# Kernel optimization log

Hardware: AMD Instinct MI355X
Metric: run time of the kernel (lower is better)

## Reference

```python
import jax, jax.numpy as jnp
import numpy as np

B, N, D = 8, 8192, 512
H, WIDTH = 8, 2048
DH = D // H
EPS = 1e-5


def _ln(x, g, b):
    m = jnp.mean(x, axis=-1, keepdims=True)
    v = jnp.mean(jnp.square(x - m), axis=-1, keepdims=True)
    return (x - m) * jax.lax.rsqrt(v + EPS) * g + b


def setup_inputs() -> dict:
    key = jax.random.key(0)
    ks = jax.random.split(key, 16)
    s = 0.02
    return {
        "x": jax.random.normal(ks[0], (B, N, D), dtype=jnp.float32),
        "mask": jnp.ones((B, N), dtype=jnp.float32),
        "Wq": jax.random.normal(ks[1], (D, D), dtype=jnp.float32) * s,
        "bq": jnp.zeros((D,), dtype=jnp.float32),
        "Wk": jax.random.normal(ks[2], (D, D), dtype=jnp.float32) * s,
        "bk": jnp.zeros((D,), dtype=jnp.float32),
        "Wv": jax.random.normal(ks[3], (D, D), dtype=jnp.float32) * s,
        "bv": jnp.zeros((D,), dtype=jnp.float32),
        "q_alpha": jax.random.normal(ks[4], (H, DH), dtype=jnp.float32),
        "k_beta": jax.random.normal(ks[5], (H, DH), dtype=jnp.float32),
        "Wo": jax.random.normal(ks[6], (D, D), dtype=jnp.float32) * s,
        "bo": jnp.zeros((D,), dtype=jnp.float32),
        "ln0_g": jnp.ones((D,), dtype=jnp.float32),
        "ln0_b": jnp.zeros((D,), dtype=jnp.float32),
        "ln1_g": jnp.ones((D,), dtype=jnp.float32),
        "ln1_b": jnp.zeros((D,), dtype=jnp.float32),
        "W1": jax.random.normal(ks[7], (WIDTH, D), dtype=jnp.float32) * s,
        "b1": jnp.zeros((WIDTH,), dtype=jnp.float32),
        "W2": jax.random.normal(ks[8], (D, WIDTH), dtype=jnp.float32) * s,
        "b2": jnp.zeros((D,), dtype=jnp.float32),
    }


def reference(x, mask, Wq, bq, Wk, bk, Wv, bv, q_alpha, k_beta, Wo, bo,
              ln0_g, ln0_b, ln1_g, ln1_b, W1, b1, W2, b2):
    scale = DH ** -0.5
    mask_ = mask[..., None]                       # [B,N,1]
    valid = (mask != 0)[..., None]                # [B,N,1] bool, broadcast over H

    residual = x
    xn = _ln(x, ln0_g, ln0_b) * mask_

    Q = (xn @ Wq.T + bq).reshape(B, N, H, DH)
    K = (xn @ Wk.T + bk).reshape(B, N, H, DH)
    V = (xn @ Wv.T + bv).reshape(B, N, H, DH)

    # stage 1: global query pooling
    alpha = jnp.einsum('bnhd,hd->bnh', Q, q_alpha) * scale
    alpha = jnp.where(valid, alpha, -jnp.inf)
    alpha = jax.nn.softmax(alpha, axis=1)         # softmax over N
    global_q = jnp.einsum('bnhd,bnh->bhd', Q, alpha)

    # stage 2: global value pooling
    P = K * global_q[:, None]                     # [B,N,H,DH]
    beta = jnp.einsum('bnhd,hd->bnh', P, k_beta) * scale
    beta = jnp.where(valid, beta, -jnp.inf)
    beta = jax.nn.softmax(beta, axis=1)
    global_v = jnp.einsum('bnhd,bnh->bhd', V, beta)

    out = (Q + global_v[:, None]).reshape(B, N, D)
    out = out @ Wo.T + bo
    x = residual + out

    residual = x
    xn = _ln(x, ln1_g, ln1_b)
    h = jax.nn.gelu(xn @ W1.T + b1, approximate=False)
    h = jax.nn.gelu(h @ W2.T + b2, approximate=False)
    x = residual + h
    x = x * mask_
    return x
```

## Files before the change

kernel.cpp:

```cpp
#include <hip/hip_runtime.h>
#include <hip/hip_bf16.h>
#include <math.h>

typedef short s8v __attribute__((ext_vector_type(8)));
typedef short s4v __attribute__((ext_vector_type(4)));
typedef __bf16 bf8v __attribute__((ext_vector_type(8)));
typedef float f4v __attribute__((ext_vector_type(4)));

#define GLOBAL_AS __attribute__((address_space(1)))
#define LDS_AS __attribute__((address_space(3)))

static __device__ __forceinline__ float bf2f(ushort u) {
  return __builtin_bit_cast(float, (unsigned int)u << 16);
}
static __device__ __forceinline__ ushort f2bf(float f) {
  unsigned int u = __builtin_bit_cast(unsigned int, f);
  u += 0x7FFFu + ((u >> 16) & 1u);
  return (ushort)(u >> 16);
}
static __device__ __forceinline__ float gelu_f(float v) {
  float t = v * v;
  float u = v * (0.0356774081f * t + 0.7978845608f);
  float e = __expf(-2.0f * u);
  return v * __builtin_amdgcn_rcpf(1.0f + e);
}
static __device__ __forceinline__ float wave_max_f(float v) {
  #pragma unroll
  for (int o = 32; o >= 1; o >>= 1) v = fmaxf(v, __shfl_xor(v, o));
  return v;
}
static __device__ __forceinline__ float wave_sum_f(float v) {
  #pragma unroll
  for (int o = 32; o >= 1; o >>= 1) v += __shfl_xor(v, o);
  return v;
}
static __device__ __forceinline__ void gload16(const ushort* g, const ushort* l) {
  __builtin_amdgcn_global_load_lds(
      (const GLOBAL_AS unsigned int*)g,
      (LDS_AS unsigned int*)l, 16, 0, 0);
}

__global__ void cvt_f32_bf16(const float* __restrict__ in, ushort* __restrict__ out, int n) {
  int i = (blockIdx.x * 256 + threadIdx.x) * 4;
  if (i >= n) return;
  float4 v = *(const float4*)(in + i);
  s4v o;
  o[0] = (short)f2bf(v.x); o[1] = (short)f2bf(v.y);
  o[2] = (short)f2bf(v.z); o[3] = (short)f2bf(v.w);
  *(s4v*)(out + i) = o;
}

__global__ __launch_bounds__(256) void transpose512(
    const float* __restrict__ in, float* __restrict__ out) {
  __shared__ float t[32][33];
  const int bx = blockIdx.x & 15, by = blockIdx.x >> 4;
  const int tx = threadIdx.x & 31, ty = threadIdx.x >> 5;
  #pragma unroll
  for (int i = 0; i < 4; ++i)
    t[ty + i * 8][tx] = in[(long)(by * 32 + ty + i * 8) * 512 + bx * 32 + tx];
  __syncthreads();
  #pragma unroll
  for (int i = 0; i < 4; ++i)
    out[(long)(bx * 32 + ty + i * 8) * 512 + by * 32 + tx] = t[tx][ty + i * 8];
}

__global__ __launch_bounds__(256) void wqo_kernel(
    const float* __restrict__ Wo, const float* __restrict__ Wq,
    ushort* __restrict__ WqoB)
{
  __shared__ float lO[64][33];
  __shared__ float lQ[32][65];
  const int t = threadIdx.x;
  const int bi = (blockIdx.x & 7) * 64, bj = (blockIdx.x >> 3) * 64;
  float acc[16] = {};
  for (int k0 = 0; k0 < 512; k0 += 32) {
    __syncthreads();
    {
      const int r = t >> 2, c = (t & 3) * 8;
      #pragma unroll
      for (int j = 0; j < 8; ++j) lO[r][c + j] = Wo[(long)(bi + r) * 512 + k0 + c + j];
      const int r2 = t >> 3, c2 = (t & 7) * 8;
      #pragma unroll
      for (int j = 0; j < 8; ++j) lQ[r2][c2 + j] = Wq[(long)(k0 + r2) * 512 + bj + c2 + j];
    }
    __syncthreads();
    const int j = t & 63, ig = t >> 6;
    for (int kk = 0; kk < 32; ++kk) {
      float q = lQ[kk][j];
      #pragma unroll
      for (int ii = 0; ii < 16; ++ii) acc[ii] += lO[ig * 16 + ii][kk] * q;
    }
  }
  const int j = t & 63, ig = t >> 6;
  #pragma unroll
  for (int ii = 0; ii < 16; ++ii)
    WqoB[(long)(bi + ig * 16 + ii) * 512 + bj + j] = f2bf(acc[ii]);
}

__global__ __launch_bounds__(256) void wa_kernel(
    const float* __restrict__ qa, const float* __restrict__ Wq,
    const float* __restrict__ bqv, ushort* __restrict__ waB, float* __restrict__ ca)
{
  __shared__ float ql[64];
  const int h = blockIdx.x;
  const int t = threadIdx.x;
  if (h >= 8) {
    waB[h * 512 + t] = 0; waB[h * 512 + 256 + t] = 0;
    if (t == 0) ca[h] = 0.f;
    return;
  }
  if (t < 64) ql[t] = qa[h * 64 + t];
  __syncthreads();
  #pragma unroll
  for (int half = 0; half < 2; ++half) {
    const int k = half * 256 + t;
    float s = 0;
    for (int dd = 0; dd < 64; ++dd) s += ql[dd] * Wq[(long)(h * 64 + dd) * 512 + k];
    waB[h * 512 + k] = f2bf(s);
  }
  if (t == 0) {
    float s = 0;
    for (int dd = 0; dd < 64; ++dd) s += ql[dd] * bqv[h * 64 + dd];
    ca[h] = s;
  }
}

__global__ __launch_bounds__(256) void ln_rows(
    const float* __restrict__ x, const float* __restrict__ gam,
    const float* __restrict__ bet, const float* __restrict__ mask,
    ushort* __restrict__ out)
{
  const int tid = threadIdx.x, lane = tid & 63, wv = tid >> 6;
  const long row = (long)blockIdx.x * 4 + wv;
  const float* xp = x + row * 512 + lane * 8;
  float4 a = *(const float4*)xp;
  float4 b = *(const float4*)(xp + 4);
  float s = a.x + a.y + a.z + a.w + b.x + b.y + b.z + b.w;
  float q = a.x*a.x + a.y*a.y + a.z*a.z + a.w*a.w
          + b.x*b.x + b.y*b.y + b.z*b.z + b.w*b.w;
  s = wave_sum_f(s); q = wave_sum_f(q);
  float m = s * (1.f / 512.f);
  float var = q * (1.f / 512.f) - m * m;
  float r = rsqrtf(var + 1e-5f);
  float mk = mask ? mask[row] : 1.f;
  const float* gp = gam + lane * 8;
  const float* bp = bet + lane * 8;
  float4 g0 = *(const float4*)gp, g1 = *(const float4*)(gp + 4);
  float4 c0 = *(const float4*)bp, c1 = *(const float4*)(bp + 4);
  s8v o;
  o[0] = (short)f2bf(((a.x - m) * r * g0.x + c0.x) * mk);
  o[1] = (short)f2bf(((a.y - m) * r * g0.y + c0.y) * mk);
  o[2] = (short)f2bf(((a.z - m) * r * g0.z + c0.z) * mk);
  o[3] = (short)f2bf(((a.w - m) * r * g0.w + c0.w) * mk);
  o[4] = (short)f2bf(((b.x - m) * r * g1.x + c1.x) * mk);
  o[5] = (short)f2bf(((b.y - m) * r * g1.y + c1.y) * mk);
  o[6] = (short)f2bf(((b.z - m) * r * g1.z + c1.z) * mk);
  o[7] = (short)f2bf(((b.w - m) * r * g1.w + c1.w) * mk);
  *(s8v*)(out + row * 512 + lane * 8) = o;
}

template<int BS, int CS>
__global__ __launch_bounds__(256) void logits_k(
    const ushort* __restrict__ XN, const ushort* __restrict__ Wl,
    const float* __restrict__ cvec, const float* __restrict__ mask,
    float* __restrict__ outL)
{
  __shared__ ushort lw[16 * 512];
  const int tid = threadIdx.x, lane = tid & 63, wv = tid >> 6;
  const long r0 = (long)blockIdx.x * 64;
  const int b = (int)(r0 >> 13);
  #pragma unroll
  for (int i = 0; i < 4; ++i) {
    const int u = tid + i * 256;
    const int h2 = u >> 6, uu = u & 63;
    s8v v = *(const s8v*)(Wl + (long)b * BS + h2 * 512 + uu * 8);
    *(s8v*)(lw + h2 * 512 + (uu ^ (h2 & 7)) * 8) = v;
  }
  __syncthreads();
  const int h = lane & 15, q = lane >> 4;
  const long rw = r0 + wv * 16;
  const ushort* ap = XN + (rw + (lane & 15)) * 512 + q * 8;
  f4v acc = {};
  #pragma unroll
  for (int t = 0; t < 16; ++t) {
    bf8v a = *(const bf8v*)(ap + t * 32);
    bf8v bb = *(const bf8v*)(lw + h * 512 + (((t * 4 + q) ^ (h & 7))) * 8);
    acc = __builtin_amdgcn_mfma_f32_16x16x32_bf16(a, bb, acc, 0, 0, 0);
  }
  const float cv = cvec[b * CS + h];
  #pragma unroll
  for (int j = 0; j < 4; ++j) {
    const long n = rw + q * 4 + j;
    float v = (acc[j] + cv) * 0.125f;
    if (mask[n] == 0.f) v = -1e30f;
    if (h < 8) outL[((long)((b << 3) + h) << 13) + (n & 8191)] = v;
  }
}

__global__ __launch_bounds__(1024) void softmax_rows(float* __restrict__ L)
{
  __shared__ float red[16];
  __shared__ float bc;
  const int tid = threadIdx.x, lane = tid & 63, wv = tid >> 6;
  float* p = L + ((long)blockIdx.x << 13) + tid * 8;
  float4 v0 = *(float4*)p;
  float4 v1 = *(float4*)(p + 4);
  float m = fmaxf(fmaxf(fmaxf(v0.x, v0.y), fmaxf(v0.z, v0.w)),
                  fmaxf(fmaxf(v1.x, v1.y), fmaxf(v1.z, v1.w)));
  m = wave_max_f(m);
  if (lane == 0) red[wv] = m;
  __syncthreads();
  if (tid < 64) {
    float t = (lane < 16) ? red[lane] : -INFINITY;
    t = wave_max_f(t);
    if (lane == 0) bc = t;
  }
  __syncthreads();
  const float gm = bc;
  v0.x = __expf(v0.x - gm); v0.y = __expf(v0.y - gm);
  v0.z = __expf(v0.z - gm); v0.w = __expf(v0.w - gm);
  v1.x = __expf(v1.x - gm); v1.y = __expf(v1.y - gm);
  v1.z = __expf(v1.z - gm); v1.w = __expf(v1.w - gm);
  float s = v0.x + v0.y + v0.z + v0.w + v1.x + v1.y + v1.z + v1.w;
  s = wave_sum_f(s);
  __syncthreads();
  if (lane == 0) red[wv] = s;
  __syncthreads();
  if (tid < 64) {
    float t = (lane < 16) ? red[lane] : 0.f;
    t = wave_sum_f(t);
    if (lane == 0) bc = t;
  }
  __syncthreads();
  const float inv = 1.0f / bc;
  v0.x *= inv; v0.y *= inv; v0.z *= inv; v0.w *= inv;
  v1.x *= inv; v1.y *= inv; v1.z *= inv; v1.w *= inv;
  *(float4*)p = v0;
  *(float4*)(p + 4) = v1;
}

__global__ __launch_bounds__(256) void pool_w(
    const ushort* __restrict__ XN, const float* __restrict__ wbuf,
    float* __restrict__ part)
{
  __shared__ float wlds[128][8];
  __shared__ float cmb[4][512];
  const int tid = threadIdx.x;
  const int b = blockIdx.x >> 6, ch = blockIdx.x & 63;
  const long g0 = ((long)b << 13) + ch * 128;
  if (tid < 128) {
    #pragma unroll
    for (int h = 0; h < 8; ++h)
      wlds[tid][h] = wbuf[(((long)(b * 8 + h)) << 13) + ch * 128 + tid];
  }
  __syncthreads();
  const int rg = tid >> 6, c8 = (tid & 63) * 8;
  f4v acc[8][2] = {};
  for (int it = 0; it < 32; ++it) {
    const int r = it * 4 + rg;
    s8v xv = *(const s8v*)(XN + (g0 + r) * 512 + c8);
    float xf[8];
    #pragma unroll
    for (int j = 0; j < 8; ++j) xf[j] = bf2f((ushort)xv[j]);
    #pragma unroll
    for (int h = 0; h < 8; ++h) {
      const float w = wlds[r][h];
      #pragma unroll
      for (int j = 0; j < 8; ++j) acc[h][j >> 2][j & 3] += w * xf[j];
    }
  }
  #pragma unroll
  for (int h = 0; h < 8; ++h) {
    __syncthreads();
    #pragma unroll
    for (int j = 0; j < 8; ++j) cmb[rg][c8 + j] = acc[h][j >> 2][j & 3];
    __syncthreads();
    const int col = tid * 2;
    float s0 = cmb[0][col] + cmb[1][col] + cmb[2][col] + cmb[3][col];
    float s1 = cmb[0][col + 1] + cmb[1][col + 1] + cmb[2][col + 1] + cmb[3][col + 1];
    *(float2*)(part + (((long)blockIdx.x * 8 + h) << 9) + col) = make_float2(s0, s1);
  }
}

__global__ __launch_bounds__(256) void combine_px(
    const float* __restrict__ part, float* __restrict__ px)
{
  const int bh = blockIdx.x;
  const int b = bh >> 3, h = bh & 7;
  const int col = threadIdx.x * 2;
  float s0 = 0.f, s1 = 0.f;
  for (int ch = 0; ch < 64; ++ch) {
    const float* p = part + (((long)((b * 64 + ch) * 8 + h)) << 9) + col;
    s0 += p[0]; s1 += p[1];
  }
  px[(bh << 9) + col] = s0;
  px[(bh << 9) + col + 1] = s1;
}

__global__ __launch_bounds__(64) void prep_gq_wb(
    const float* __restrict__ px, const float* __restrict__ WqT,
    const float* __restrict__ bqv, const float* __restrict__ kbv,
    const float* __restrict__ Wk, const float* __restrict__ bkv,
    ushort* __restrict__ wbB, float* __restrict__ cbs)
{
  __shared__ float pxl[512];
  __shared__ float gkb[64];
  const int bh = blockIdx.x, b = bh >> 3, h = bh & 7, d = threadIdx.x;
  #pragma unroll
  for (int i = 0; i < 8; ++i) pxl[d + i * 64] = px[(bh << 9) + d + i * 64];
  __syncthreads();
  float acc = bqv[h * 64 + d];
  for (int c = 0; c < 512; ++c) acc += pxl[c] * WqT[(long)c * 512 + h * 64 + d];
  gkb[d] = acc * kbv[h * 64 + d];
  __syncthreads();
  float s[8] = {};
  for (int dd = 0; dd < 64; ++dd) {
    const float g = gkb[dd];
    const float* wr = Wk + (long)(h * 64 + dd) * 512 + d;
    #pragma unroll
    for (int ki = 0; ki < 8; ++ki) s[ki] += g * wr[ki * 64];
  }
  #pragma unroll
  for (int ki = 0; ki < 8; ++ki)
    wbB[(long)(b * 16 + h) * 512 + d + ki * 64] = f2bf(s[ki]);
  if (d == 0) {
    float t = 0.f;
    for (int dd = 0; dd < 64; ++dd) t += gkb[dd] * bkv[h * 64 + dd];
    cbs[b * 16 + h] = t;
  }
  if (h == 0) {
    #pragma unroll
    for (int hp = 8; hp < 16; ++hp)
      for (int k = d; k < 512; k += 64) wbB[(long)(b * 16 + hp) * 512 + k] = 0;
    if (d < 8) cbs[b * 16 + 8 + d] = 0.f;
  }
}

__global__ __launch_bounds__(64) void prep_gv(
    const float* __restrict__ pv, const float* __restrict__ WvT,
    const float* __restrict__ bvv, const float* __restrict__ bqv,
    float* __restrict__ gvb)
{
  __shared__ float pxl[512];
  const int bh = blockIdx.x, b = bh >> 3, h = bh & 7, d = threadIdx.x;
  #pragma unroll
  for (int i = 0; i < 8; ++i) pxl[d + i * 64] = pv[(bh << 9) + d + i * 64];
  __syncthreads();
  float acc = bvv[h * 64 + d] + bqv[h * 64 + d];
  for (int c = 0; c < 512; ++c) acc += pxl[c] * WvT[(long)c * 512 + h * 64 + d];
  gvb[b * 512 + h * 64 + d] = acc;
}

__global__ __launch_bounds__(256) void bias_gv(
    const float* __restrict__ gv, const float* __restrict__ Wo,
    const float* __restrict__ bo, float* __restrict__ bo2) {
  const int b = blockIdx.x;
  const int n = blockIdx.y * 256 + threadIdx.x;
  const float* g = gv + b * 512;
  const float* w = Wo + (long)n * 512;
  float acc = 0.f;
  for (int d = 0; d < 512; d += 4) {
    float4 wv4 = *(const float4*)(w + d);
    acc += g[d] * wv4.x + g[d + 1] * wv4.y + g[d + 2] * wv4.z + g[d + 3] * wv4.w;
  }
  bo2[b * 512 + n] = bo[n] + acc;
}

#define MFMA_(d,a,b) d = __builtin_amdgcn_mfma_f32_16x16x32_bf16(a, b, d, 0, 0, 0)

template<int EPI, int LDA, int NN, int KK>
__global__ __launch_bounds__(512, 2) void gemm256(
    const ushort* __restrict__ A, const ushort* __restrict__ W,
    const float* __restrict__ bias, const float* __restrict__ resid,
    const float* __restrict__ mask, void* __restrict__ Out)
{
  constexpr int NBX = NN / 256;
  constexpr int NT = KK / 64;
  __shared__ __align__(16) ushort lds[2][2][16384];
  const int tid = threadIdx.x;
  const int lane = tid & 63;
  const int w = tid >> 6;
  const int wm = w >> 2, wn = w & 3;

  const int nwg = gridDim.x;
  const int cpx = nwg >> 3;
  const int wg = (blockIdx.x & 7) * cpx + (blockIdx.x >> 3);
  const int bx = wg % NBX, by = wg / NBX;
  const long bm = (long)by * 256;
  const int bn = bx * 256;

  const int srow = tid >> 3;
  const int sku = (tid & 7) ^ (srow & 7);
  const ushort* aln[4];
  const ushort* bln[4];
  #pragma unroll
  for (int l = 0; l < 4; ++l) {
    aln[l] = A + (bm + l * 64 + srow) * (long)LDA + sku * 8;
    bln[l] = W + (long)(bn + l * 64 + srow) * KK + sku * 8;
  }

#define STG_A(bf_, l_, Tt) gload16(aln[l_] + (Tt) * 64, &lds[bf_][0][(l_) * 4096 + w * 512])
#define STG_B(bf_, l_, Tt) gload16(bln[l_] + (Tt) * 64, &lds[bf_][1][(l_) * 4096 + w * 512])

  STG_B(0, 0, 0); STG_B(0, 1, 0);
  STG_B(0, 2, 0); STG_B(0, 3, 0);
  STG_A(0, 0, 0); STG_A(0, 2, 0);
  STG_A(0, 1, 0); STG_A(0, 3, 0);

  f4v acc[8][4] = {};

  const int s0 = ((lane >> 4) ^ (lane & 7)) * 8;
  const int s1 = ((4 + (lane >> 4)) ^ (lane & 7)) * 8;
  const int ar = (wm * 128 + (lane & 15)) * 64;
  const int br = (wn * 64 + (lane & 15)) * 64;

  asm volatile("s_waitcnt vmcnt(2)" ::: "memory");
  asm volatile("s_barrier" ::: "memory");

  for (int T = 0; T < NT; ++T) {
    const int buf = T & 1, nb = buf ^ 1;
    const ushort* LA = &lds[buf][0][0];
    const ushort* LB = &lds[buf][1][0];
    const bool st = (T + 1 < NT);
    bf8v aR[8], bR[8];
    #pragma unroll
    for (int m = 0; m < 4; ++m) {
      aR[2 * m]     = *(const bf8v*)(LA + ar + m * 1024 + s0);
      aR[2 * m + 1] = *(const bf8v*)(LA + ar + m * 1024 + s1);
    }
    #pragma unroll
    for (int n = 0; n < 2; ++n) {
      bR[2 * n]     = *(const bf8v*)(LB + br + n * 1024 + s0);
      bR[2 * n + 1] = *(const bf8v*)(LB + br + n * 1024 + s1);
    }
    if (st) { STG_B(nb, 0, T + 1); STG_B(nb, 1, T + 1); }
    asm volatile("s_barrier" ::: "memory");
    __builtin_amdgcn_s_setprio(1);
    #pragma unroll
    for (int m = 0; m < 4; ++m)
      #pragma unroll
      for (int n = 0; n < 2; ++n) {
        MFMA_(acc[m][n], aR[2 * m], bR[2 * n]);
        MFMA_(acc[m][n], aR[2 * m + 1], bR[2 * n + 1]);
      }
    __builtin_amdgcn_s_setprio(0);
    #pragma unroll
    for (int n = 2; n < 4; ++n) {
      bR[2 * n]     = *(const bf8v*)(LB + br + n * 1024 + s0);
      bR[2 * n + 1] = *(const bf8v*)(LB + br + n * 1024 + s1);
    }
    if (st) { STG_B(nb, 2, T + 1); STG_B(nb, 3, T + 1); }
    if (st) asm volatile("s_waitcnt vmcnt(4)" ::: "memory");
    else    asm volatile("s_waitcnt vmcnt(0)" ::: "memory");
    asm volatile("s_barrier" ::: "memory");
    __builtin_amdgcn_s_setprio(1);
    #pragma unroll
    for (int m = 0; m < 4; ++m)
      #pragma unroll
      for (int n = 2; n < 4; ++n) {
        MFMA_(acc[m][n], aR[2 * m], bR[2 * n]);
        MFMA_(acc[m][n], aR[2 * m + 1], bR[2 * n + 1]);
      }
    __builtin_amdgcn_s_setprio(0);
    #pragma unroll
    for (int m = 0; m < 4; ++m) {
      aR[2 * m]     = *(const bf8v*)(LA + ar + (m + 4) * 1024 + s0);
      aR[2 * m + 1] = *(const bf8v*)(LA + ar + (m + 4) * 1024 + s1);
    }
    if (st) { STG_A(nb, 0, T + 1); STG_A(nb, 2, T + 1); }
    asm volatile("s_barrier" ::: "memory");
    __builtin_amdgcn_s_setprio(1);
    #pragma unroll
    for (int m = 0; m < 4; ++m)
      #pragma unroll
      for (int n = 0; n < 2; ++n) {
        MFMA_(acc[m + 4][n], aR[2 * m], bR[2 * n]);
        MFMA_(acc[m + 4][n], aR[2 * m + 1], bR[2 * n + 1]);
      }
    __builtin_amdgcn_s_setprio(0);
    if (st) { STG_A(nb, 1, T + 1); STG_A(nb, 3, T + 1); }
    asm volatile("s_waitcnt vmcnt(2)" ::: "memory");
    asm volatile("s_barrier" ::: "memory");
    __builtin_amdgcn_s_setprio(1);
    #pragma unroll
    for (int m = 0; m < 4; ++m)
      #pragma unroll
      for (int n = 2; n < 4; ++n) {
        MFMA_(acc[m + 4][n], aR[2 * m], bR[2 * n]);
        MFMA_(acc[m + 4][n], aR[2 * m + 1], bR[2 * n + 1]);
      }
    __builtin_amdgcn_s_setprio(0);
  }
#undef STG_A
#undef STG_B

  const int colbase = bn + wn * 64 + (lane & 15);
  const long rowb0 = bm + wm * 128 + ((lane >> 4) * 4);
  const float* biasp = (EPI == 4) ? bias + ((bm >> 13) << 9) : bias;
  #pragma unroll
  for (int m = 0; m < 8; ++m) {
    #pragma unroll
    for (int j = 0; j < 4; ++j) {
      const long row = rowb0 + m * 16 + j;
      #pragma unroll
      for (int n = 0; n < 4; ++n) {
        const int col = colbase + n * 16;
        float v = acc[m][n][j] + biasp[col];
        const long idx = row * (long)NN + col;
        if constexpr (EPI == 0) {
          ((ushort*)Out)[idx] = f2bf(v);
        } else if constexpr (EPI == 2) {
          ((ushort*)Out)[idx] = f2bf(gelu_f(v));
        } else if constexpr (EPI == 3) {
          ((float*)Out)[idx] = (resid[idx] + gelu_f(v)) * mask[row];
        } else {
          ((float*)Out)[idx] = v + resid[idx];
        }
      }
    }
  }
}

extern "C" void kernel_launch(void* const* d_in, const int* in_sizes, int n_in,
                              void* d_out, int out_size, void* d_ws, size_t ws_size,
                              hipStream_t stream) {
  const float* x    = (const float*)d_in[0];
  const float* mask = (const float*)d_in[1];
  const float* Wq   = (const float*)d_in[2];
  const float* bq   = (const float*)d_in[3];
  const float* Wk   = (const float*)d_in[4];
  const float* bk   = (const float*)d_in[5];
  const float* Wv   = (const float*)d_in[6];
  const float* bv   = (const float*)d_in[7];
  const float* qa   = (const float*)d_in[8];
  const float* kb   = (const float*)d_in[9];
  const float* Wo   = (const float*)d_in[10];
  const float* bo   = (const float*)d_in[11];
  const float* g0   = (const float*)d_in[12];
  const float* be0  = (const float*)d_in[13];
  const float* g1   = (const float*)d_in[14];
  const float* be1  = (const float*)d_in[15];
  const float* W1   = (const float*)d_in[16];
  const float* b1   = (const float*)d_in[17];
  const float* W2   = (const float*)d_in[18];
  const float* b2   = (const float*)d_in[19];
  float* out = (float*)d_out;

  const int M = 65536;
  char* ws = (char*)d_ws;
  const size_t MB = 1024 * 1024;
  ushort* XN  = (ushort*)(ws);
  float*  X1  = (float*)(ws + 64 * MB);
  ushort* H1  = (ushort*)(ws + 192 * MB);
  float*  AL  = (float*)(ws + 192 * MB);
  float*  BL  = (float*)(ws + 194 * MB);
  float*  PART= (float*)(ws + 196 * MB);
  char* base = ws + 448 * MB;
  ushort* W1B  = (ushort*)(base);
  ushort* W2B  = (ushort*)(base + 2 * MB);
  ushort* WqoB = (ushort*)(base + 4 * MB);
  float*  WqT  = (float*)(base + 4 * MB + 512 * 1024);
  float*  WvT  = (float*)(base + 5 * MB + 512 * 1024);
  ushort* waB  = (ushort*)(base + 6 * MB + 512 * 1024);
  ushort* wbB  = (ushort*)(base + 6 * MB + 528 * 1024);
  float*  ca   = (float*)(base + 6 * MB + 656 * 1024);
  float*  cbs  = (float*)(base + 6 * MB + 660 * 1024);
  float*  PX   = (float*)(base + 6 * MB + 664 * 1024);
  float*  PV   = (float*)(base + 6 * MB + 792 * 1024);
  float*  GVB  = (float*)(base + 6 * MB + 920 * 1024);
  float*  BO2  = (float*)(base + 6 * MB + 936 * 1024);

  cvt_f32_bf16<<<1024, 256, 0, stream>>>(W1, W1B, 1048576);
  cvt_f32_bf16<<<1024, 256, 0, stream>>>(W2, W2B, 1048576);
  wqo_kernel<<<64, 256, 0, stream>>>(Wo, Wq, WqoB);
  wa_kernel<<<16, 256, 0, stream>>>(qa, Wq, bq, waB, ca);
  transpose512<<<256, 256, 0, stream>>>(Wq, WqT);
  transpose512<<<256, 256, 0, stream>>>(Wv, WvT);

  ln_rows<<<M / 4, 256, 0, stream>>>(x, g0, be0, mask, XN);

  logits_k<0, 0><<<1024, 256, 0, stream>>>(XN, waB, ca, mask, AL);
  softmax_rows<<<64, 1024, 0, stream>>>(AL);
  pool_w<<<512, 256, 0, stream>>>(XN, AL, PART);
  combine_px<<<64, 256, 0, stream>>>(PART, PX);
  prep_gq_wb<<<64, 64, 0, stream>>>(PX, WqT, bq, kb, Wk, bk, wbB, cbs);

  logits_k<8192, 16><<<1024, 256, 0, stream>>>(XN, wbB, cbs, mask, BL);
  softmax_rows<<<64, 1024, 0, stream>>>(BL);
  pool_w<<<512, 256, 0, stream>>>(XN, BL, PART);
  combine_px<<<64, 256, 0, stream>>>(PART, PV);
  prep_gv<<<64, 64, 0, stream>>>(PV, WvT, bv, bq, GVB);
  bias_gv<<<dim3(8, 2), 256, 0, stream>>>(GVB, Wo, bo, BO2);

  gemm256<4, 512, 512, 512><<<2 * (M / 256), 512, 0, stream>>>(
      XN, WqoB, BO2, x, nullptr, X1);

  ln_rows<<<M / 4, 256, 0, stream>>>(X1, g1, be1, nullptr, XN);

  gemm256<2, 512, 2048, 512><<<8 * (M / 256), 512, 0, stream>>>(
      XN, W1B, b1, nullptr, nullptr, H1);
  gemm256<3, 2048, 512, 2048><<<2 * (M / 256), 512, 0, stream>>>(
      H1, W2B, b2, X1, mask, out);
}
```

Baseline: 703.1 us.

## Shrink GEMM tiles to 128x256 with K=32 steps and store X1 as bf16

The three big GEMMs move from a 256x256 tile with K-step 64 and 64KB LDS to a 128x256 tile with K-step 32 and a single combined LDS buffer. Launch bounds now allow four workgroups per CU, aiming for higher occupancy and better latency hiding. The intermediate residual X1 is now stored as bf16 instead of fp32, with a new bf16 LayerNorm kernel, to cut memory traffic. In exchange, each loaded tile is reused less, there are more barriers per unit of work, and the residual path loses precision.

```diff
diff --git a/kernel.cpp b/kernel.cpp
--- a/kernel.cpp
+++ b/kernel.cpp
@@ -159,6 +159,35 @@
   *(s8v*)(out + row * 512 + lane * 8) = o;
 }
 
+__global__ __launch_bounds__(256) void ln_rows_bf16(
+    const ushort* __restrict__ x, const float* __restrict__ gam,
+    const float* __restrict__ bet, ushort* __restrict__ out)
+{
+  const int tid = threadIdx.x, lane = tid & 63, wv = tid >> 6;
+  const long row = (long)blockIdx.x * 4 + wv;
+  s8v v = *(const s8v*)(x + row * 512 + lane * 8);
+  float xv[8];
+  #pragma unroll
+  for (int j = 0; j < 8; ++j) xv[j] = bf2f((ushort)v[j]);
+  float s = 0.f, q = 0.f;
+  #pragma unroll
+  for (int j = 0; j < 8; ++j) { s += xv[j]; q += xv[j] * xv[j]; }
+  s = wave_sum_f(s); q = wave_sum_f(q);
+  float m = s * (1.f / 512.f);
+  float var = q * (1.f / 512.f) - m * m;
+  float r = rsqrtf(var + 1e-5f);
+  const float* gp = gam + lane * 8;
+  const float* bp = bet + lane * 8;
+  float4 g0 = *(const float4*)gp, g1 = *(const float4*)(gp + 4);
+  float4 c0 = *(const float4*)bp, c1 = *(const float4*)(bp + 4);
+  float gg[8] = {g0.x, g0.y, g0.z, g0.w, g1.x, g1.y, g1.z, g1.w};
+  float cc[8] = {c0.x, c0.y, c0.z, c0.w, c1.x, c1.y, c1.z, c1.w};
+  s8v o;
+  #pragma unroll
+  for (int j = 0; j < 8; ++j) o[j] = (short)f2bf((xv[j] - m) * r * gg[j] + cc[j]);
+  *(s8v*)(out + row * 512 + lane * 8) = o;
+}
+
 template<int BS, int CS>
 __global__ __launch_bounds__(256) void logits_k(
     const ushort* __restrict__ XN, const ushort* __restrict__ Wl,
@@ -369,14 +398,14 @@
 #define MFMA_(d,a,b) d = __builtin_amdgcn_mfma_f32_16x16x32_bf16(a, b, d, 0, 0, 0)
 
 template<int EPI, int LDA, int NN, int KK>
-__global__ __launch_bounds__(512, 2) void gemm256(
+__global__ __launch_bounds__(512, 4) void gemmP(
     const ushort* __restrict__ A, const ushort* __restrict__ W,
-    const float* __restrict__ bias, const float* __restrict__ resid,
+    const float* __restrict__ bias, const void* __restrict__ resid,
     const float* __restrict__ mask, void* __restrict__ Out)
 {
   constexpr int NBX = NN / 256;
-  constexpr int NT = KK / 64;
-  __shared__ __align__(16) ushort lds[2][2][16384];
+  constexpr int NT = KK / 32;
+  __shared__ __align__(16) ushort lds[2][12288];
   const int tid = threadIdx.x;
   const int lane = tid & 63;
   const int w = tid >> 6;
@@ -386,135 +415,93 @@
   const int cpx = nwg >> 3;
   const int wg = (blockIdx.x & 7) * cpx + (blockIdx.x >> 3);
   const int bx = wg % NBX, by = wg / NBX;
-  const long bm = (long)by * 256;
+  const long bm = (long)by * 128;
   const int bn = bx * 256;
 
-  const int srow = tid >> 3;
-  const int sku = (tid & 7) ^ (srow & 7);
-  const ushort* aln[4];
-  const ushort* bln[4];
-  #pragma unroll
-  for (int l = 0; l < 4; ++l) {
-    aln[l] = A + (bm + l * 64 + srow) * (long)LDA + sku * 8;
-    bln[l] = W + (long)(bn + l * 64 + srow) * KK + sku * 8;
-  }
-
-#define STG_A(bf_, l_, Tt) gload16(aln[l_] + (Tt) * 64, &lds[bf_][0][(l_) * 4096 + w * 512])
-#define STG_B(bf_, l_, Tt) gload16(bln[l_] + (Tt) * 64, &lds[bf_][1][(l_) * 4096 + w * 512])
-
-  STG_B(0, 0, 0); STG_B(0, 1, 0);
-  STG_B(0, 2, 0); STG_B(0, 3, 0);
-  STG_A(0, 0, 0); STG_A(0, 2, 0);
-  STG_A(0, 1, 0); STG_A(0, 3, 0);
-
-  f4v acc[8][4] = {};
-
-  const int s0 = ((lane >> 4) ^ (lane & 7)) * 8;
-  const int s1 = ((4 + (lane >> 4)) ^ (lane & 7)) * 8;
-  const int ar = (wm * 128 + (lane & 15)) * 64;
-  const int br = (wn * 64 + (lane & 15)) * 64;
-
-  asm volatile("s_waitcnt vmcnt(2)" ::: "memory");
+  const int scr = tid >> 2, sls = tid & 3;
+  const int akU = ((sls ^ (scr & 3) ^ ((scr >> 2) & 3))) * 8;
+  const ushort* asrc = A + (bm + scr) * (long)LDA + akU;
+  const int rbe = (scr & 31) + ((scr >> 5) << 6);
+  const ushort* besrc = W + (long)(bn + rbe) * KK + akU;
+  const ushort* bosrc = W + (long)(bn + rbe + 32) * KK + akU;
+
+#define STG_A(nb_, Tt)  gload16(asrc + (Tt) * 32, &lds[nb_][tid * 8])
+#define STG_BE(nb_, Tt) gload16(besrc + (Tt) * 32, &lds[nb_][4096 + tid * 8])
+#define STG_BO(nb_, Tt) gload16(bosrc + (Tt) * 32, &lds[nb_][8192 + tid * 8])
+
+  STG_A(0, 0); STG_BE(0, 0); STG_BO(0, 0);
+
+  f4v acc[4][4] = {};
+
+  const int L = lane & 15, q = lane >> 4;
+  const int soff = (q ^ (lane & 3) ^ ((lane >> 2) & 3)) * 8;
+  const int abase = (wm * 64 + L) * 32 + soff;
+  const int bbase = 4096 + (wn * 32 + L) * 32 + soff;
+
+  asm volatile("s_waitcnt vmcnt(1)" ::: "memory");
   asm volatile("s_barrier" ::: "memory");
 
   for (int T = 0; T < NT; ++T) {
     const int buf = T & 1, nb = buf ^ 1;
-    const ushort* LA = &lds[buf][0][0];
-    const ushort* LB = &lds[buf][1][0];
+    const ushort* Lp = &lds[buf][0];
     const bool st = (T + 1 < NT);
-    bf8v aR[8], bR[8];
-    #pragma unroll
-    for (int m = 0; m < 4; ++m) {
-      aR[2 * m]     = *(const bf8v*)(LA + ar + m * 1024 + s0);
-      aR[2 * m + 1] = *(const bf8v*)(LA + ar + m * 1024 + s1);
-    }
-    #pragma unroll
-    for (int n = 0; n < 2; ++n) {
-      bR[2 * n]     = *(const bf8v*)(LB + br + n * 1024 + s0);
-      bR[2 * n + 1] = *(const bf8v*)(LB + br + n * 1024 + s1);
-    }
-    if (st) { STG_B(nb, 0, T + 1); STG_B(nb, 1, T + 1); }
+    bf8v aR[4], bR[4];
+    #pragma unroll
+    for (int m = 0; m < 4; ++m) aR[m] = *(const bf8v*)(Lp + abase + m * 512);
+    bR[0] = *(const bf8v*)(Lp + bbase);
+    bR[1] = *(const bf8v*)(Lp + bbase + 512);
+    if (st) {
+      STG_A(nb, T + 1); STG_BE(nb, T + 1);
+      asm volatile("s_waitcnt vmcnt(2)" ::: "memory");
+    } else {
+      asm volatile("s_waitcnt vmcnt(0)" ::: "memory");
+    }
     asm volatile("s_barrier" ::: "memory");
     __builtin_amdgcn_s_setprio(1);
     #pragma unroll
-    for (int m = 0; m < 4; ++m)
-      #pragma unroll
-      for (int n = 0; n < 2; ++n) {
-        MFMA_(acc[m][n], aR[2 * m], bR[2 * n]);
-        MFMA_(acc[m][n], aR[2 * m + 1], bR[2 * n + 1]);
-      }
+    for (int m = 0; m < 4; ++m) {
+      MFMA_(acc[m][0], aR[m], bR[0]);
+      MFMA_(acc[m][1], aR[m], bR[1]);
+    }
     __builtin_amdgcn_s_setprio(0);
-    #pragma unroll
-    for (int n = 2; n < 4; ++n) {
-      bR[2 * n]     = *(const bf8v*)(LB + br + n * 1024 + s0);
-      bR[2 * n + 1] = *(const bf8v*)(LB + br + n * 1024 + s1);
-    }
-    if (st) { STG_B(nb, 2, T + 1); STG_B(nb, 3, T + 1); }
-    if (st) asm volatile("s_waitcnt vmcnt(4)" ::: "memory");
-    else    asm volatile("s_waitcnt vmcnt(0)" ::: "memory");
+    bR[2] = *(const bf8v*)(Lp + bbase + 4096);
+    bR[3] = *(const bf8v*)(Lp + bbase + 4096 + 512);
+    if (st) {
+      STG_BO(nb, T + 1);
+      asm volatile("s_waitcnt vmcnt(1)" ::: "memory");
+    }
     asm volatile("s_barrier" ::: "memory");
     __builtin_amdgcn_s_setprio(1);
     #pragma unroll
-    for (int m = 0; m < 4; ++m)
-      #pragma unroll
-      for (int n = 2; n < 4; ++n) {
-        MFMA_(acc[m][n], aR[2 * m], bR[2 * n]);
-        MFMA_(acc[m][n], aR[2 * m + 1], bR[2 * n + 1]);
-      }
+    for (int m = 0; m < 4; ++m) {
+      MFMA_(acc[m][2], aR[m], bR[2]);
+      MFMA_(acc[m][3], aR[m], bR[3]);
+    }
     __builtin_amdgcn_s_setprio(0);
-    #pragma unroll
-    for (int m = 0; m < 4; ++m) {
-      aR[2 * m]     = *(const bf8v*)(LA + ar + (m + 4) * 1024 + s0);
-      aR[2 * m + 1] = *(const bf8v*)(LA + ar + (m + 4) * 1024 + s1);
-    }
-    if (st) { STG_A(nb, 0, T + 1); STG_A(nb, 2, T + 1); }
-    asm volatile("s_barrier" ::: "memory");
-    __builtin_amdgcn_s_setprio(1);
-    #pragma unroll
-    for (int m = 0; m < 4; ++m)
-      #pragma unroll
-      for (int n = 0; n < 2; ++n) {
-        MFMA_(acc[m + 4][n], aR[2 * m], bR[2 * n]);
-        MFMA_(acc[m + 4][n], aR[2 * m + 1], bR[2 * n + 1]);
-      }
-    __builtin_amdgcn_s_setprio(0);
-    if (st) { STG_A(nb, 1, T + 1); STG_A(nb, 3, T + 1); }
-    asm volatile("s_waitcnt vmcnt(2)" ::: "memory");
-    asm volatile("s_barrier" ::: "memory");
-    __builtin_amdgcn_s_setprio(1);
-    #pragma unroll
-    for (int m = 0; m < 4; ++m)
-      #pragma unroll
-      for (int n = 2; n < 4; ++n) {
-        MFMA_(acc[m + 4][n], aR[2 * m], bR[2 * n]);
-        MFMA_(acc[m + 4][n], aR[2 * m + 1], bR[2 * n + 1]);
-      }
-    __builtin_amdgcn_s_setprio(0);
   }
 #undef STG_A
-#undef STG_B
-
-  const int colbase = bn + wn * 64 + (lane & 15);
-  const long rowb0 = bm + wm * 128 + ((lane >> 4) * 4);
-  const float* biasp = (EPI == 4) ? bias + ((bm >> 13) << 9) : bias;
-  #pragma unroll
-  for (int m = 0; m < 8; ++m) {
+#undef STG_BE
+#undef STG_BO
+
+  const int colb = bn + wn * 64 + L;
+  const long rowb = bm + wm * 64 + q * 4;
+  const float* biasp = (EPI == 5) ? bias + ((bm >> 13) << 9) : bias;
+  #pragma unroll
+  for (int m = 0; m < 4; ++m) {
     #pragma unroll
     for (int j = 0; j < 4; ++j) {
-      const long row = rowb0 + m * 16 + j;
+      const long row = rowb + m * 16 + j;
       #pragma unroll
       for (int n = 0; n < 4; ++n) {
-        const int col = colbase + n * 16;
+        const int col = colb + n * 16;
         float v = acc[m][n][j] + biasp[col];
         const long idx = row * (long)NN + col;
-        if constexpr (EPI == 0) {
-          ((ushort*)Out)[idx] = f2bf(v);
-        } else if constexpr (EPI == 2) {
+        if constexpr (EPI == 2) {
           ((ushort*)Out)[idx] = f2bf(gelu_f(v));
         } else if constexpr (EPI == 3) {
-          ((float*)Out)[idx] = (resid[idx] + gelu_f(v)) * mask[row];
+          ((float*)Out)[idx] = (bf2f(((const ushort*)resid)[idx]) + gelu_f(v)) * mask[row];
         } else {
-          ((float*)Out)[idx] = v + resid[idx];
+          ((ushort*)Out)[idx] = f2bf(v + ((const float*)resid)[idx]);
         }
       }
     }
@@ -550,7 +537,7 @@
   char* ws = (char*)d_ws;
   const size_t MB = 1024 * 1024;
   ushort* XN  = (ushort*)(ws);
-  float*  X1  = (float*)(ws + 64 * MB);
+  ushort* X1  = (ushort*)(ws + 64 * MB);
   ushort* H1  = (ushort*)(ws + 192 * MB);
   float*  AL  = (float*)(ws + 192 * MB);
   float*  BL  = (float*)(ws + 194 * MB);
@@ -592,13 +579,13 @@
   prep_gv<<<64, 64, 0, stream>>>(PV, WvT, bv, bq, GVB);
   bias_gv<<<dim3(8, 2), 256, 0, stream>>>(GVB, Wo, bo, BO2);
 
-  gemm256<4, 512, 512, 512><<<2 * (M / 256), 512, 0, stream>>>(
+  gemmP<5, 512, 512, 512><<<2 * (M / 128), 512, 0, stream>>>(
       XN, WqoB, BO2, x, nullptr, X1);
 
-  ln_rows<<<M / 4, 256, 0, stream>>>(X1, g1, be1, nullptr, XN);
-
-  gemm256<2, 512, 2048, 512><<<8 * (M / 256), 512, 0, stream>>>(
+  ln_rows_bf16<<<M / 4, 256, 0, stream>>>(X1, g1, be1, XN);
+
+  gemmP<2, 512, 2048, 512><<<8 * (M / 128), 512, 0, stream>>>(
       XN, W1B, b1, nullptr, nullptr, H1);
-  gemm256<3, 2048, 512, 2048><<<2 * (M / 256), 512, 0, stream>>>(
+  gemmP<3, 2048, 512, 2048><<<2 * (M / 128), 512, 0, stream>>>(
       H1, W2B, b2, X1, mask, out);
 }
```

After: 712.2 us. No clear change (+1.3%).
